# Kernel optimization log

Hardware: AMD Instinct MI355X
Metric: run time of the kernel (lower is better)

The kernel has to match this reference:

```python
import jax, jax.numpy as jnp
import numpy as np
from jax import lax

B, C_IN, H, W = 8, 64, 256, 256
C_OUT = 128
M = 800000      # number of pixel mappings
V = 200000      # number of views (atomic groups)
N = 50000       # number of 3D points (view groups)


def _csr_ptr(key, n_seg, total):
    inner = jnp.sort(jax.random.randint(key, (n_seg - 1,), 0, total + 1, dtype=jnp.int32))
    return jnp.concatenate([jnp.zeros((1,), jnp.int32), inner,
                            jnp.full((1,), total, jnp.int32)])


def setup_inputs() -> dict:
    key = jax.random.key(0)
    k = jax.random.split(key, 7)
    x = jax.random.normal(k[0], (B, C_IN, H, W), jnp.float32)
    w = jax.random.normal(k[1], (C_OUT, C_IN, 3, 3), jnp.float32) * (1.0 / np.sqrt(C_IN * 9))
    b = jax.random.normal(k[2], (C_OUT,), jnp.float32) * 0.01
    x_3d = jax.random.normal(k[3], (N, C_OUT), jnp.float32)
    n_flat = B * (H // 2) * (W // 2)  # flattened down-conv output pixels
    fm_idx = jax.random.randint(k[4], (M,), 0, n_flat, dtype=jnp.int32)
    a_ptr = _csr_ptr(k[5], V, M)
    v_ptr = _csr_ptr(k[6], N, V)
    return {"x": x, "w": w, "b": b, "x_3d": x_3d,
            "fm_idx": fm_idx, "a_ptr": a_ptr, "v_ptr": v_ptr}


def _csr_segment_max(feats, ptr, num_segments):
    # CSR pointers -> per-row segment ids (jit-safe), then segment max.
    seg = jnp.searchsorted(ptr, jnp.arange(feats.shape[0], dtype=ptr.dtype), side='right') - 1
    out = jax.ops.segment_max(feats, seg, num_segments=num_segments)
    return jnp.where(jnp.isfinite(out), out, 0.0)  # empty segments -> 0


def reference(x, w, b, x_3d, fm_idx, a_ptr, v_ptr):
    # conv down (stride 2, pad 1) + ReLU
    y = lax.conv_general_dilated(x, w, (2, 2), ((1, 1), (1, 1)),
                                 dimension_numbers=('NCHW', 'OIHW', 'NCHW'))
    y = jax.nn.relu(y + b[None, :, None, None])
    # feature map indexing: flat gather of mapped pixels -> [M, C]
    flat = y.transpose(0, 2, 3, 1).reshape(-1, y.shape[1])
    g = flat[fm_idx]
    # atomic pool: pixels -> views (CSR segment max)
    xv = _csr_segment_max(g, a_ptr, V)
    # view pool: views -> 3D points (CSR segment max)
    xp = _csr_segment_max(xv, v_ptr, N)
    # additive fusion
    return x_3d + xp
```

## Files before the change

### kernel.cpp

```cpp
#include <hip/hip_runtime.h>
#include <hip/hip_bf16.h>


#define B_IMG  8
#define C_IN   64
#define H_IN   256
#define W_IN   256
#define C_OUT  128
#define OH     128
#define OW     128
#define NPIX   (B_IMG * OH * OW)
#define KTOT   576
#define N_PTS  50000

#define HP     258
#define PLANE  (129 * 64)
#define HROW   (2 * PLANE)

typedef __bf16 bf16x8 __attribute__((ext_vector_type(8)));
typedef float  f32x4  __attribute__((ext_vector_type(4)));

typedef unsigned int __attribute__((address_space(3))) u32_lds;
typedef unsigned int __attribute__((address_space(1))) u32_glb;

#define GLOAD_LDS16(gsrc, ldst)                                                \
  __builtin_amdgcn_global_load_lds((const u32_glb*)(gsrc),                     \
                                   (u32_lds*)(ldst), 16, 0, 0)

#define XTP_BYTES   (B_IMG * HP * HROW * 2)
#define G_BYTES     (NPIX * C_OUT * 2)
#define XTP_OFF     0
#define G_OFF       XTP_BYTES
#define WT2_OFF     (XTP_BYTES + G_BYTES)

__global__ __launch_bounds__(256) void halo_zero_kernel(__hip_bfloat16* __restrict__ xtp) {
  const int ph = blockIdx.x;
  const int b  = blockIdx.y;
  const int tid = threadIdx.x;
  const long base = ((long)b * HP + ph) * HROW;
  uint4 z = make_uint4(0u, 0u, 0u, 0u);
  uint4* p = (uint4*)(xtp + base);
  if (ph == 0 || ph == HP - 1) {
    for (int i = tid; i < (HROW * 2) / 16; i += 256) p[i] = z;
  } else {
    if (tid < 8) p[tid] = z;
    else if (tid < 16) ((uint4*)(xtp + base + PLANE + 128 * 64))[tid - 8] = z;
  }
}

__global__ __launch_bounds__(256) void transpose_x_kernel(
    const float* __restrict__ x, unsigned* __restrict__ xtp32) {
  __shared__ unsigned tile32[32][65];
  const int tid = threadIdx.x;
  const int w0  = blockIdx.x * 64;
  const int h   = blockIdx.y;
  const int b   = blockIdx.z;

  const int wl = tid & 63;
  const int c4 = tid >> 6;
  for (int cc = 0; cc < 8; ++cc) {
    int cpair = cc * 4 + c4;
    const float* xr = x + (((long)(b * C_IN + 2 * cpair) * H_IN) + h) * W_IN + w0;
    float v0 = xr[wl];
    float v1 = xr[(long)H_IN * W_IN + wl];
    unsigned u0 = __builtin_bit_cast(unsigned short, (__bf16)v0);
    unsigned u1 = __builtin_bit_cast(unsigned short, (__bf16)v1);
    tile32[cpair][wl] = u0 | (u1 << 16);
  }
  __syncthreads();
  const int cpair = tid & 31;
  const int ws0   = tid >> 5;
  const long rowb2 = (((long)(b * HP) + h + 1) * HROW) >> 1;
  for (int it = 0; it < 8; ++it) {
    int wloc = it * 8 + ws0;
    int pc   = w0 + wloc + 1;
    xtp32[rowb2 + (pc & 1) * (PLANE >> 1) + (pc >> 1) * 32 + cpair] =
        tile32[cpair][wloc];
  }
}

__global__ __launch_bounds__(256) void wprep_kernel(
    const float* __restrict__ w, __hip_bfloat16* __restrict__ wt2b) {
  int tid  = blockIdx.x * 256 + threadIdx.x;
  int khkw = tid >> 13;
  int cout = (tid >> 6) & 127;
  int ci   = tid & 63;
  wt2b[tid] = (__hip_bfloat16)w[(cout * C_IN + ci) * 9 + khkw];
}

__global__ __launch_bounds__(512) void conv_gemm_kernel(
    const __hip_bfloat16* __restrict__ xtp,
    const __hip_bfloat16* __restrict__ wt2b,
    const float* __restrict__ bias,
    __hip_bfloat16* __restrict__ g) {
  __shared__ __hip_bfloat16 Abuf[2][8192];
  __shared__ __hip_bfloat16 Bbuf[2][8192];

  const int tid  = threadIdx.x;
  const int lane = tid & 63;
  const int wid  = tid >> 6;
  const int bid  = blockIdx.x;
  const int bimg = bid >> 7;
  const int oh   = bid & 127;
  const int wr   = wid >> 2;
  const int wc   = wid & 3;

  f32x4 acc[4][2] = {};

  auto stage = [&](int buf, int t) {
    const int kh = t / 3;
    const int kw = t - kh * 3;
    const long abase = (((long)bimg * HP + (2 * oh + kh)) * 2 + (kw & 1)) * PLANE
                       + ((kw == 2) ? 64 : 0);
    const long bbase = (long)t * 8192;
    for (int p = 0; p < 2; ++p) {
      int flat = p * 512 + tid;
      int row  = flat >> 3;
      int cs   = (flat & 7) ^ (row & 7);
      long soff = (long)row * 64 + cs * 8;
      char* dA = (char*)&Abuf[buf][0] + flat * 16;
      char* dB = (char*)&Bbuf[buf][0] + flat * 16;
      GLOAD_LDS16(xtp + abase + soff, dA);
      GLOAD_LDS16(wt2b + bbase + soff, dB);
    }
  };

  auto compute = [&](int buf) {
    const int r15 = lane & 15;
    const int kg  = lane >> 4;
    for (int h = 0; h < 2; ++h) {
      bf16x8 af[4], bfv[2];
      const int co = h * 4 + kg;
      for (int i = 0; i < 4; ++i) {
        int rowa = wr * 64 + i * 16 + r15;
        int ca   = co ^ (rowa & 7);
        af[i] = *(const bf16x8*)((const char*)&Abuf[buf][0] + rowa * 128 + ca * 16);
      }
      for (int n = 0; n < 2; ++n) {
        int rowb = wc * 32 + n * 16 + r15;
        int cb   = co ^ (rowb & 7);
        bfv[n] = *(const bf16x8*)((const char*)&Bbuf[buf][0] + rowb * 128 + cb * 16);
      }
      for (int i = 0; i < 4; ++i)
        for (int n = 0; n < 2; ++n)
          acc[i][n] = __builtin_amdgcn_mfma_f32_16x16x32_bf16(af[i], bfv[n],
                                                              acc[i][n], 0, 0, 0);
    }
  };

  stage(0, 0);
  __syncthreads();
  int cur = 0;
  for (int t = 0; t < 9; ++t) {
    if (t + 1 < 9) stage(cur ^ 1, t + 1);
    compute(cur);
    __syncthreads();
    cur ^= 1;
  }

  __hip_bfloat16* ct = &Abuf[0][0];
  const int col0 = wc * 32 + (lane & 15);
  float bn[2];
  for (int n = 0; n < 2; ++n) bn[n] = bias[col0 + n * 16];
  for (int i = 0; i < 4; ++i) {
    int row0 = wr * 64 + i * 16 + (lane >> 4) * 4;
    for (int n = 0; n < 2; ++n) {
      int cout = col0 + n * 16;
      for (int r = 0; r < 4; ++r) {
        float v = fmaxf(acc[i][n][r] + bn[n], 0.0f);
        ct[(row0 + r) * 128 + cout] = (__hip_bfloat16)v;
      }
    }
  }
  __syncthreads();
  const long gbase = (long)bid * (128 * 128);
  for (int it = 0; it < 4; ++it) {
    int flat = it * 512 + tid;
    bf16x8 v = *(const bf16x8*)((const char*)ct + flat * 16);
    *(bf16x8*)(g + gbase + (long)flat * 8) = v;
  }
}

__global__ __launch_bounds__(256) void gather_max_add_kernel(
    const __hip_bfloat16* __restrict__ g,
    const float* __restrict__ x3d,
    const int* __restrict__ fm_idx,
    const int* __restrict__ a_ptr,
    const int* __restrict__ v_ptr,
    float* __restrict__ out) {
  __shared__ float red[4][128];
  const int tid  = threadIdx.x;
  const int lane = tid & 63;
  const int wid  = tid >> 6;
  const int n    = blockIdx.x;

  const int v0 = v_ptr[n];
  const int v1 = v_ptr[n + 1];
  const int r0 = a_ptr[v0];
  const int r1 = a_ptr[v1];
  const int len = r1 - r0;

  const int sub  = lane >> 4;
  const int ch16 = lane & 15;

  float m[8];
#pragma unroll
  for (int k = 0; k < 8; ++k) m[k] = 0.0f;

  const uint4* gp = (const uint4*)g;

  for (int base = wid * 64; base < len; base += 256) {
    int nb = len - base;
    if (nb > 64) nb = 64;
    int li = base + lane;
    if (li >= len) li = len - 1;
    const int idx_l = fm_idx[r0 + li];

    for (int j = 0; j < nb; j += 8) {
      int ra = j + sub;
      int rb = j + 4 + sub;
      if (ra >= nb) ra = nb - 1;
      if (rb >= nb) rb = nb - 1;
      int ia = __shfl(idx_l, ra);
      int ib = __shfl(idx_l, rb);
      uint4 va = gp[(long)ia * 16 + ch16];
      uint4 vb = gp[(long)ib * 16 + ch16];
      const unsigned* ua = (const unsigned*)&va;
      const unsigned* ub = (const unsigned*)&vb;
#pragma unroll
      for (int w = 0; w < 4; ++w) {
        m[2 * w]     = fmaxf(m[2 * w],     __uint_as_float(ua[w] << 16));
        m[2 * w + 1] = fmaxf(m[2 * w + 1], __uint_as_float(ua[w] & 0xffff0000u));
        m[2 * w]     = fmaxf(m[2 * w],     __uint_as_float(ub[w] << 16));
        m[2 * w + 1] = fmaxf(m[2 * w + 1], __uint_as_float(ub[w] & 0xffff0000u));
      }
    }
  }

#pragma unroll
  for (int k = 0; k < 8; ++k) {
    m[k] = fmaxf(m[k], __shfl_xor(m[k], 16));
    m[k] = fmaxf(m[k], __shfl_xor(m[k], 32));
  }
  if (sub == 0) {
#pragma unroll
    for (int k = 0; k < 8; ++k) red[wid][ch16 * 8 + k] = m[k];
  }
  __syncthreads();

  if (tid < 128) {
    float v = fmaxf(fmaxf(red[0][tid], red[1][tid]),
                    fmaxf(red[2][tid], red[3][tid]));
    out[(long)n * 128 + tid] = x3d[(long)n * 128 + tid] + v;
  }
}

extern "C" void kernel_launch(void* const* d_in, const int* in_sizes, int n_in,
                              void* d_out, int out_size, void* d_ws, size_t ws_size,
                              hipStream_t stream) {
  const float* x     = (const float*)d_in[0];
  const float* w     = (const float*)d_in[1];
  const float* bias  = (const float*)d_in[2];
  const float* x3d   = (const float*)d_in[3];
  const int*   fmidx = (const int*)d_in[4];
  const int*   aptr  = (const int*)d_in[5];
  const int*   vptr  = (const int*)d_in[6];
  float* out = (float*)d_out;

  char* ws = (char*)d_ws;
  __hip_bfloat16* xtp  = (__hip_bfloat16*)(ws + XTP_OFF);
  __hip_bfloat16* g    = (__hip_bfloat16*)(ws + G_OFF);
  __hip_bfloat16* wt2b = (__hip_bfloat16*)(ws + WT2_OFF);

  hipLaunchKernelGGL(halo_zero_kernel, dim3(HP, B_IMG), dim3(256), 0, stream,
                     xtp);
  hipLaunchKernelGGL(transpose_x_kernel, dim3(W_IN / 64, H_IN, B_IMG), dim3(256),
                     0, stream, x, (unsigned*)xtp);
  hipLaunchKernelGGL(wprep_kernel, dim3((C_OUT * KTOT) / 256), dim3(256), 0,
                     stream, w, wt2b);
  hipLaunchKernelGGL(conv_gemm_kernel, dim3(NPIX / 128), dim3(512), 0, stream,
                     xtp, wt2b, bias, g);
  hipLaunchKernelGGL(gather_max_add_kernel, dim3(N_PTS), dim3(256), 0,
                     stream, g, x3d, fmidx, aptr, vptr, out);
}
```

Before: 346.0 us.

## Retile conv GEMM to 4 waves with deeper prefetch and wave-per-point gather

The conv GEMM moves to 256 threads, each wave computing a 64x64 tile (4x4 MFMA accumulators). It prefetches two k-steps ahead using explicit vmcnt waits and raw barriers, and remaps block IDs to interleave images. The gather/max kernel now assigns one wave per 3D point, dropping the LDS cross-wave reduction and barrier, and issues four gathered loads per iteration with vectorized x3d/output access. This targets GEMM pipeline stalls and per-block sync overhead, at the cost of more registers and less parallelism within long segments.

```diff
diff --git a/kernel.cpp b/kernel.cpp
--- a/kernel.cpp
+++ b/kernel.cpp
@@ -88,7 +88,7 @@
   wt2b[tid] = (__hip_bfloat16)w[(cout * C_IN + ci) * 9 + khkw];
 }
 
-__global__ __launch_bounds__(512) void conv_gemm_kernel(
+__global__ __launch_bounds__(256) void conv_gemm_kernel(
     const __hip_bfloat16* __restrict__ xtp,
     const __hip_bfloat16* __restrict__ wt2b,
     const float* __restrict__ bias,
@@ -99,13 +99,14 @@
   const int tid  = threadIdx.x;
   const int lane = tid & 63;
   const int wid  = tid >> 6;
-  const int bid  = blockIdx.x;
+  const int b0   = blockIdx.x;
+  const int bid  = (b0 & 7) * 128 + (b0 >> 3);
   const int bimg = bid >> 7;
   const int oh   = bid & 127;
-  const int wr   = wid >> 2;
-  const int wc   = wid & 3;
-
-  f32x4 acc[4][2] = {};
+  const int wr   = wid >> 1;
+  const int wc   = wid & 1;
+
+  f32x4 acc[4][4] = {};
 
   auto stage = [&](int buf, int t) {
     const int kh = t / 3;
@@ -113,8 +114,9 @@
     const long abase = (((long)bimg * HP + (2 * oh + kh)) * 2 + (kw & 1)) * PLANE
                        + ((kw == 2) ? 64 : 0);
     const long bbase = (long)t * 8192;
-    for (int p = 0; p < 2; ++p) {
-      int flat = p * 512 + tid;
+#pragma unroll
+    for (int p = 0; p < 4; ++p) {
+      int flat = p * 256 + tid;
       int row  = flat >> 3;
       int cs   = (flat & 7) ^ (row & 7);
       long soff = (long)row * 64 + cs * 8;
@@ -128,43 +130,52 @@
   auto compute = [&](int buf) {
     const int r15 = lane & 15;
     const int kg  = lane >> 4;
+#pragma unroll
     for (int h = 0; h < 2; ++h) {
-      bf16x8 af[4], bfv[2];
+      bf16x8 af[4], bfv[4];
       const int co = h * 4 + kg;
+#pragma unroll
       for (int i = 0; i < 4; ++i) {
         int rowa = wr * 64 + i * 16 + r15;
         int ca   = co ^ (rowa & 7);
         af[i] = *(const bf16x8*)((const char*)&Abuf[buf][0] + rowa * 128 + ca * 16);
-      }
-      for (int n = 0; n < 2; ++n) {
-        int rowb = wc * 32 + n * 16 + r15;
+        int rowb = wc * 64 + i * 16 + r15;
         int cb   = co ^ (rowb & 7);
-        bfv[n] = *(const bf16x8*)((const char*)&Bbuf[buf][0] + rowb * 128 + cb * 16);
-      }
+        bfv[i] = *(const bf16x8*)((const char*)&Bbuf[buf][0] + rowb * 128 + cb * 16);
+      }
+#pragma unroll
       for (int i = 0; i < 4; ++i)
-        for (int n = 0; n < 2; ++n)
+#pragma unroll
+        for (int n = 0; n < 4; ++n)
           acc[i][n] = __builtin_amdgcn_mfma_f32_16x16x32_bf16(af[i], bfv[n],
                                                               acc[i][n], 0, 0, 0);
     }
   };
 
   stage(0, 0);
-  __syncthreads();
-  int cur = 0;
+  stage(1, 1);
+#pragma unroll 1
   for (int t = 0; t < 9; ++t) {
-    if (t + 1 < 9) stage(cur ^ 1, t + 1);
-    compute(cur);
-    __syncthreads();
-    cur ^= 1;
+    if (t < 8) {
+      asm volatile("s_waitcnt vmcnt(8)" ::: "memory");
+    } else {
+      asm volatile("s_waitcnt vmcnt(0)" ::: "memory");
+    }
+    __builtin_amdgcn_sched_barrier(0);
+    __builtin_amdgcn_s_barrier();
+    compute(t & 1);
+    __builtin_amdgcn_s_barrier();
+    __builtin_amdgcn_sched_barrier(0);
+    if (t + 2 < 9) stage(t & 1, t + 2);
   }
 
   __hip_bfloat16* ct = &Abuf[0][0];
-  const int col0 = wc * 32 + (lane & 15);
-  float bn[2];
-  for (int n = 0; n < 2; ++n) bn[n] = bias[col0 + n * 16];
+  const int col0 = wc * 64 + (lane & 15);
+  float bn[4];
+  for (int n = 0; n < 4; ++n) bn[n] = bias[col0 + n * 16];
   for (int i = 0; i < 4; ++i) {
     int row0 = wr * 64 + i * 16 + (lane >> 4) * 4;
-    for (int n = 0; n < 2; ++n) {
+    for (int n = 0; n < 4; ++n) {
       int cout = col0 + n * 16;
       for (int r = 0; r < 4; ++r) {
         float v = fmaxf(acc[i][n][r] + bn[n], 0.0f);
@@ -174,8 +185,8 @@
   }
   __syncthreads();
   const long gbase = (long)bid * (128 * 128);
-  for (int it = 0; it < 4; ++it) {
-    int flat = it * 512 + tid;
+  for (int it = 0; it < 8; ++it) {
+    int flat = it * 256 + tid;
     bf16x8 v = *(const bf16x8*)((const char*)ct + flat * 16);
     *(bf16x8*)(g + gbase + (long)flat * 8) = v;
   }
@@ -188,11 +199,8 @@
     const int* __restrict__ a_ptr,
     const int* __restrict__ v_ptr,
     float* __restrict__ out) {
-  __shared__ float red[4][128];
-  const int tid  = threadIdx.x;
-  const int lane = tid & 63;
-  const int wid  = tid >> 6;
-  const int n    = blockIdx.x;
+  const int lane = threadIdx.x & 63;
+  const int n    = blockIdx.x * 4 + (threadIdx.x >> 6);
 
   const int v0 = v_ptr[n];
   const int v1 = v_ptr[n + 1];
@@ -203,36 +211,45 @@
   const int sub  = lane >> 4;
   const int ch16 = lane & 15;
 
+  const float4* x4 = (const float4*)x3d;
+  const long b0 = (long)n * 32 + ch16 * 2;
+  float4 xa, xb;
+  if (sub == 0) { xa = x4[b0]; xb = x4[b0 + 1]; }
+
   float m[8];
 #pragma unroll
   for (int k = 0; k < 8; ++k) m[k] = 0.0f;
 
   const uint4* gp = (const uint4*)g;
 
-  for (int base = wid * 64; base < len; base += 256) {
+  for (int base = 0; base < len; base += 64) {
     int nb = len - base;
     if (nb > 64) nb = 64;
     int li = base + lane;
     if (li >= len) li = len - 1;
     const int idx_l = fm_idx[r0 + li];
 
-    for (int j = 0; j < nb; j += 8) {
-      int ra = j + sub;
-      int rb = j + 4 + sub;
-      if (ra >= nb) ra = nb - 1;
-      if (rb >= nb) rb = nb - 1;
-      int ia = __shfl(idx_l, ra);
-      int ib = __shfl(idx_l, rb);
-      uint4 va = gp[(long)ia * 16 + ch16];
-      uint4 vb = gp[(long)ib * 16 + ch16];
-      const unsigned* ua = (const unsigned*)&va;
-      const unsigned* ub = (const unsigned*)&vb;
-#pragma unroll
-      for (int w = 0; w < 4; ++w) {
-        m[2 * w]     = fmaxf(m[2 * w],     __uint_as_float(ua[w] << 16));
-        m[2 * w + 1] = fmaxf(m[2 * w + 1], __uint_as_float(ua[w] & 0xffff0000u));
-        m[2 * w]     = fmaxf(m[2 * w],     __uint_as_float(ub[w] << 16));
-        m[2 * w + 1] = fmaxf(m[2 * w + 1], __uint_as_float(ub[w] & 0xffff0000u));
+    for (int j = 0; j < nb; j += 16) {
+      int r[4];
+#pragma unroll
+      for (int q = 0; q < 4; ++q) {
+        int rr = j + q * 4 + sub;
+        r[q] = (rr >= nb) ? nb - 1 : rr;
+      }
+      uint4 v[4];
+#pragma unroll
+      for (int q = 0; q < 4; ++q) {
+        int iq = __shfl(idx_l, r[q]);
+        v[q] = gp[(long)iq * 16 + ch16];
+      }
+#pragma unroll
+      for (int q = 0; q < 4; ++q) {
+        const unsigned* u = (const unsigned*)&v[q];
+#pragma unroll
+        for (int w = 0; w < 4; ++w) {
+          m[2 * w]     = fmaxf(m[2 * w],     __uint_as_float(u[w] << 16));
+          m[2 * w + 1] = fmaxf(m[2 * w + 1], __uint_as_float(u[w] & 0xffff0000u));
+        }
       }
     }
   }
@@ -242,16 +259,14 @@
     m[k] = fmaxf(m[k], __shfl_xor(m[k], 16));
     m[k] = fmaxf(m[k], __shfl_xor(m[k], 32));
   }
+
   if (sub == 0) {
-#pragma unroll
-    for (int k = 0; k < 8; ++k) red[wid][ch16 * 8 + k] = m[k];
-  }
-  __syncthreads();
-
-  if (tid < 128) {
-    float v = fmaxf(fmaxf(red[0][tid], red[1][tid]),
-                    fmaxf(red[2][tid], red[3][tid]));
-    out[(long)n * 128 + tid] = x3d[(long)n * 128 + tid] + v;
+    float4* o4 = (float4*)out;
+    float4 oa, ob;
+    oa.x = xa.x + m[0]; oa.y = xa.y + m[1]; oa.z = xa.z + m[2]; oa.w = xa.w + m[3];
+    ob.x = xb.x + m[4]; ob.y = xb.y + m[5]; ob.z = xb.z + m[6]; ob.w = xb.w + m[7];
+    o4[b0]     = oa;
+    o4[b0 + 1] = ob;
   }
 }
 
@@ -278,8 +293,8 @@
                      0, stream, x, (unsigned*)xtp);
   hipLaunchKernelGGL(wprep_kernel, dim3((C_OUT * KTOT) / 256), dim3(256), 0,
                      stream, w, wt2b);
-  hipLaunchKernelGGL(conv_gemm_kernel, dim3(NPIX / 128), dim3(512), 0, stream,
+  hipLaunchKernelGGL(conv_gemm_kernel, dim3(NPIX / 128), dim3(256), 0, stream,
                      xtp, wt2b, bias, g);
-  hipLaunchKernelGGL(gather_max_add_kernel, dim3(N_PTS), dim3(256), 0,
+  hipLaunchKernelGGL(gather_max_add_kernel, dim3(N_PTS / 4), dim3(256), 0,
                      stream, g, x3d, fmidx, aptr, vptr, out);
 }
```

Measured after the change: 303.8 us. 12.2% less time.
